# Kernel tuning notes

Hardware: AMD Instinct MI355X
Metric: run time of the kernel (lower is better)

Reference implementation:

```python
import jax, jax.numpy as jnp
import numpy as np

M, K, N = 4096, 4096, 11008  # tokens, in_features, out_features
PACK = 8  # int4 nibbles per int32


def setup_inputs() -> dict:
    key = jax.random.key(0)
    k1, k2, k3, k4, k5 = jax.random.split(key, 5)
    x = jax.random.normal(k1, (M, K), dtype=jnp.float32)
    weights = jax.random.randint(k2, (N, K // PACK), 0, 2147483647, dtype=jnp.int32)
    # positive per-channel scales, small float zero offsets (GPTQ-style affine)
    scales = jax.random.uniform(k3, (N,), dtype=jnp.float32, minval=0.005, maxval=0.02)
    zeros = jax.random.normal(k4, (N,), dtype=jnp.float32) * 0.05
    bias = jax.random.normal(k5, (N,), dtype=jnp.float32) * 0.02
    return {"x": x, "weights": weights, "scales": scales, "zeros": zeros, "bias": bias}


def _unpack_int4(weights):
    # weights: [N, K//8] int32 -> nibbles [N, K] in [0, 15]
    shifts = jnp.arange(PACK, dtype=jnp.int32) * 4  # [8]
    nib = (weights[:, :, None] >> shifts[None, None, :]) & 0xF  # [N, K//8, 8]
    return nib.reshape(weights.shape[0], -1)  # [N, K]


def reference(x, weights, scales, zeros, bias):
    x_dtype = x.dtype
    xb = x.astype(jnp.bfloat16)
    q = _unpack_int4(weights).astype(jnp.bfloat16)  # [N, K]
    # dequant: w = q * scale + zero  (per output channel)
    w = q * scales.astype(jnp.bfloat16)[:, None] + zeros.astype(jnp.bfloat16)[:, None]
    out = jnp.einsum('mk,nk->mn', xb, w, preferred_element_type=jnp.float32)
    out = out + bias[None, :]
    return out.astype(x_dtype)
```

## Files before the change

kernel.cpp:

```cpp
#include <hip/hip_runtime.h>
#include <stdint.h>

#define MDIM 4096
#define KDIM 4096
#define NDIM 11008
#define KP   (KDIM/8)
#define NQB  (NDIM*KP/256)

typedef float  f32x4   __attribute__((ext_vector_type(4)));
typedef __bf16 bf16x8  __attribute__((ext_vector_type(8)));
typedef unsigned short u16x8 __attribute__((ext_vector_type(8)));
typedef int    i32x4   __attribute__((ext_vector_type(4)));
typedef int    i32x16  __attribute__((ext_vector_type(16)));
typedef char   c8x8    __attribute__((ext_vector_type(8)));
typedef char   c8x16   __attribute__((ext_vector_type(16)));

__device__ __forceinline__ unsigned short f2bf(float f) {
  uint32_t u = __builtin_bit_cast(uint32_t, f);
  u += 0x7FFFu + ((u >> 16) & 1u);
  return (unsigned short)(u >> 16);
}
__device__ __forceinline__ float bf2f(unsigned short h) {
  return __builtin_bit_cast(float, (uint32_t)h << 16);
}
__device__ __forceinline__ float bf16r(float f) { return bf2f(f2bf(f)); }

__device__ __forceinline__ void lds16(const void* g, void* l) {
  __builtin_amdgcn_global_load_lds(
      (const __attribute__((address_space(1))) unsigned int*)g,
      (__attribute__((address_space(3))) unsigned int*)l, 16, 0, 0);
}

__global__ __launch_bounds__(256) void prepass_kernel(
    const uint32_t* __restrict__ wq, c8x8* __restrict__ Q8,
    const float* __restrict__ x, c8x16* __restrict__ X8,
    float* __restrict__ delta, float* __restrict__ xsum) {
  __shared__ float red[256];
  const int blk = blockIdx.x, t = threadIdx.x;
  if (blk < NQB) {
    int idx = blk * 256 + t;
    uint32_t w = wq[idx];
    c8x8 v;
#pragma unroll
    for (int j = 0; j < 8; ++j) v[j] = (char)((w >> (4 * j)) & 0xF);
    Q8[idx] = v;
    return;
  }
  const int row = blk - NQB;
  const float4* xr = (const float4*)(x + (size_t)row * KDIM);
  float xb[16];
#pragma unroll
  for (int i = 0; i < 4; ++i) {
    float4 f = xr[t * 4 + i];
    xb[i * 4 + 0] = bf16r(f.x); xb[i * 4 + 1] = bf16r(f.y);
    xb[i * 4 + 2] = bf16r(f.z); xb[i * 4 + 3] = bf16r(f.w);
  }
  float mx = 0.f, sm = 0.f;
#pragma unroll
  for (int j = 0; j < 16; ++j) { mx = fmaxf(mx, fabsf(xb[j])); sm += xb[j]; }
  red[t] = mx; __syncthreads();
  for (int o = 128; o > 0; o >>= 1) {
    if (t < o) red[t] = fmaxf(red[t], red[t + o]);
    __syncthreads();
  }
  const float rmx = red[0];
  __syncthreads();
  red[t] = sm; __syncthreads();
  for (int o = 128; o > 0; o >>= 1) {
    if (t < o) red[t] += red[t + o];
    __syncthreads();
  }
  const float rsm = red[0];
  const float inv = (rmx > 0.f) ? 127.0f / rmx : 0.f;
  if (t == 0) {
    delta[row] = (rmx > 0.f) ? rmx / 127.0f : 0.f;
    xsum[row]  = rsm;
  }
  c8x16 q;
#pragma unroll
  for (int j = 0; j < 16; ++j) q[j] = (char)__float2int_rn(xb[j] * inv);
  X8[(size_t)row * 256 + t] = q;
}

__global__ __launch_bounds__(512, 2) void gemm256_i8_kernel(
    const char* __restrict__ A8, const char* __restrict__ Q8,
    const float* __restrict__ delta, const float* __restrict__ xsum,
    const float* __restrict__ scales, const float* __restrict__ zeros,
    const float* __restrict__ bias, float* __restrict__ out) {
  __shared__ __align__(16) char smem[131072];

  const int tid  = threadIdx.x;
  const int lane = tid & 63;
  const int wave = tid >> 6;
  const int wm   = wave >> 2;
  const int wn   = wave & 3;

  const int b   = blockIdx.x;
  const int swz = (b & 7) * 86 + (b >> 3);
  const int mt  = swz / 43;
  const int nt  = swz - mt * 43;
  const int bm0 = mt * 256, bn0 = nt * 256;

  const int srow   = lane >> 2;
  const int schunk = lane & 3;
  const int perm0  = schunk ^ (((srow >> 3) & 1) << 1);
  const int perm1  = perm0 ^ 1;
  const char* aR  = A8 + (size_t)(bm0 + wave * 32 + srow) * KDIM + perm0 * 16;
  const char* aR2 = A8 + (size_t)(bm0 + wave * 32 + 16 + srow) * KDIM + perm1 * 16;
  const char* bR  = Q8 + (size_t)(bn0 + wave * 32 + srow) * KDIM + perm0 * 16;
  const char* bR2 = Q8 + (size_t)(bn0 + wave * 32 + 16 + srow) * KDIM + perm1 * 16;

  const int r31 = lane & 31;
  const int sub = r31 >> 4;
  const int r15 = r31 & 15;
  const int hk  = lane >> 5;
  const int rd0 = sub * 1024 + r15 * 64 + ((hk ^ sub) << 4) + ((r15 & 8) << 2);
  const int rd1 = rd0 ^ 32;

  const int aoffc = wm * 8192;
  const int boffc = 65536 + wn * 4096;

  i32x16 acc[4][2];
#pragma unroll
  for (int i = 0; i < 4; ++i)
#pragma unroll
    for (int j = 0; j < 2; ++j)
#pragma unroll
      for (int r = 0; r < 16; ++r) acc[i][j][r] = 0;

  i32x4 Af[4], Bf[2];

#define STAGE_A(tile, h, slot)                                              \
  do {                                                                      \
    const size_t ko_ = (size_t)((tile) * 128 + (h) * 64);                   \
    char* d_ = smem + ((slot) << 14) + wave * 2048;                         \
    lds16(aR + ko_, d_);                                                    \
    lds16(aR2 + ko_, d_ + 1024);                                            \
  } while (0)

#define STAGE_B(tile, h, slot)                                              \
  do {                                                                      \
    const size_t ko_ = (size_t)((tile) * 128 + (h) * 64);                   \
    char* d_ = smem + 65536 + ((slot) << 14) + wave * 2048;                 \
    lds16(bR + ko_, d_);                                                    \
    lds16(bR2 + ko_, d_ + 1024);                                            \
  } while (0)

#define READ6(slotbase, S)                                                  \
  do {                                                                      \
    const int ro_ = (S) ? rd1 : rd0;                                        \
    _Pragma("unroll") for (int mf = 0; mf < 4; ++mf)                        \
        Af[mf] = *(const i32x4*)(smem + aoffc + (slotbase) +                \
                                 mf * 2048 + ro_);                          \
    _Pragma("unroll") for (int nf = 0; nf < 2; ++nf)                        \
        Bf[nf] = *(const i32x4*)(smem + boffc + (slotbase) +                \
                                 nf * 2048 + ro_);                          \
  } while (0)

#define MFMA8()                                                             \
  __builtin_amdgcn_s_setprio(1);                                            \
  _Pragma("unroll") for (int mf = 0; mf < 4; ++mf)                          \
      _Pragma("unroll") for (int nf = 0; nf < 2; ++nf)                      \
          acc[mf][nf] = __builtin_amdgcn_mfma_i32_32x32x32_i8(              \
              Af[mf], Bf[nf], acc[mf][nf], 0, 0, 0);                        \
  __builtin_amdgcn_s_setprio(0);

#define BAR                                                                 \
  __builtin_amdgcn_s_barrier();                                             \
  __builtin_amdgcn_sched_barrier(0);

#define VMWAIT(N) asm volatile("s_waitcnt vmcnt(" #N ")" ::: "memory")

#define TILE(T, S0s, S1s, SN1s, NSTG, VM1STMT, VM3STMT)                     \
  do {                                                                      \
    READ6((S0s) << 14, 0);                                                  \
    if ((NSTG) >= 1) STAGE_A((T) + 1, 1, SN1s);                             \
    BAR; MFMA8(); BAR;                                                      \
    READ6((S0s) << 14, 1);                                                  \
    if ((NSTG) >= 2) STAGE_B((T) + 1, 1, SN1s);                             \
    VM1STMT;                                                                \
    BAR; MFMA8(); BAR;                                                      \
    READ6((S1s) << 14, 0);                                                  \
    if ((NSTG) >= 3) STAGE_A((T) + 2, 0, S0s);                              \
    BAR; MFMA8(); BAR;                                                      \
    READ6((S1s) << 14, 1);                                                  \
    if ((NSTG) >= 4) STAGE_B((T) + 2, 0, S0s);                              \
    VM3STMT;                                                                \
    BAR; MFMA8(); BAR;                                                      \
  } while (0)

  STAGE_A(0, 0, 0);
  STAGE_B(0, 0, 0);
  STAGE_A(0, 1, 1);
  STAGE_B(0, 1, 1);
  STAGE_A(1, 0, 2);
  STAGE_B(1, 0, 2);
  VMWAIT(8);
  BAR;

  for (int tt = 0; tt < 30; tt += 2) {
    TILE(tt,     0, 1, 3, 4, VMWAIT(8), VMWAIT(8));
    TILE(tt + 1, 2, 3, 1, 4, VMWAIT(8), VMWAIT(8));
  }
  TILE(30, 0, 1, 3, 2, VMWAIT(8), VMWAIT(4));
  TILE(31, 2, 3, 1, 0, VMWAIT(0), (void)0);

#undef TILE
#undef VMWAIT
#undef BAR
#undef MFMA8
#undef READ6
#undef STAGE_B
#undef STAGE_A

  const int colv = bn0 + wn * 64 + (lane & 31);
  const int rowb = bm0 + wm * 128 + ((lane >> 5) << 2);
  float sb[2], zb[2], bv[2];
#pragma unroll
  for (int nf = 0; nf < 2; ++nf) {
    sb[nf] = bf16r(scales[colv + nf * 32]);
    zb[nf] = bf16r(zeros[colv + nf * 32]);
    bv[nf] = bias[colv + nf * 32];
  }
#pragma unroll
  for (int mf = 0; mf < 4; ++mf)
#pragma unroll
    for (int reg = 0; reg < 16; ++reg) {
      const int row = rowb + mf * 32 + (reg & 3) + ((reg >> 2) << 3);
      const float dm = delta[row];
      const float xm = xsum[row];
#pragma unroll
      for (int nf = 0; nf < 2; ++nf)
        out[(size_t)row * NDIM + colv + nf * 32] =
            (float)acc[mf][nf][reg] * (dm * sb[nf]) + (zb[nf] * xm + bv[nf]);
    }
}

__global__ __launch_bounds__(256, 3) void gemm_fused_kernel(
    const float* __restrict__ x, const uint32_t* __restrict__ wq,
    const float* __restrict__ scales, const float* __restrict__ zeros,
    const float* __restrict__ bias, float* __restrict__ out) {
  __shared__ __align__(16) char smem[2 * 128 * 64 * 2];
  char* As = smem;
  char* Bs = smem + 16384;

  const int tid  = threadIdx.x;
  const int lane = tid & 63;
  const int wave = tid >> 6;
  const int wm = wave >> 1, wn = wave & 1;

  const int b   = blockIdx.x;
  const int swz = (b & 7) * 344 + (b >> 3);
  const int mt  = swz / 86;
  const int nt  = swz - mt * 86;
  const int bm0 = mt * 128, bn0 = nt * 128;

  f32x4 acc[4][4];
#pragma unroll
  for (int i = 0; i < 4; ++i)
#pragma unroll
    for (int j = 0; j < 4; ++j) acc[i][j] = (f32x4){0.f, 0.f, 0.f, 0.f};

  const int base_a = ((wm * 64 + (lane & 15)) << 7) + ((lane >> 4) << 4);
  const int base_b = ((wn * 64 + (lane & 15)) << 7) + ((lane >> 4) << 4);

  float sv[4], zv[4];
#pragma unroll
  for (int it = 0; it < 4; ++it) {
    int r = bn0 + it * 32 + (tid >> 3);
    sv[it] = bf16r(scales[r]);
    zv[it] = bf16r(zeros[r]);
  }

  for (int kt = 0; kt < KDIM / 64; ++kt) {
    const int k0 = kt * 64;
    __syncthreads();
#pragma unroll
    for (int it = 0; it < 4; ++it) {
      int ch = it * 256 + tid;
      int row = ch >> 3, c8 = ch & 7;
      const float* src = x + (size_t)(bm0 + row) * KDIM + k0 + c8 * 8;
      float4 f0 = *(const float4*)src;
      float4 f1 = *(const float4*)(src + 4);
      u16x8 v;
      v[0] = f2bf(f0.x); v[1] = f2bf(f0.y); v[2] = f2bf(f0.z); v[3] = f2bf(f0.w);
      v[4] = f2bf(f1.x); v[5] = f2bf(f1.y); v[6] = f2bf(f1.z); v[7] = f2bf(f1.w);
      *(u16x8*)(As + row * 128 + c8 * 16) = v;
    }
#pragma unroll
    for (int it = 0; it < 4; ++it) {
      int ch = it * 256 + tid;
      int row = ch >> 3, kp = ch & 7;
      uint32_t w = wq[(size_t)(bn0 + row) * KP + kt * 8 + kp];
      float s = sv[it], z = zv[it];
      u16x8 v;
#pragma unroll
      for (int j = 0; j < 8; ++j) {
        float qf = (float)((w >> (4 * j)) & 0xF);
        float t  = bf16r(qf * s);
        v[j] = f2bf(t + z);
      }
      *(u16x8*)(Bs + row * 128 + kp * 16) = v;
    }
    __syncthreads();
#pragma unroll
    for (int ks = 0; ks < 2; ++ks) {
      bf16x8 af[4], bf[4];
#pragma unroll
      for (int i = 0; i < 4; ++i)
        af[i] = *(const bf16x8*)(As + base_a + i * 2048 + ks * 64);
#pragma unroll
      for (int j = 0; j < 4; ++j)
        bf[j] = *(const bf16x8*)(Bs + base_b + j * 2048 + ks * 64);
#pragma unroll
      for (int i = 0; i < 4; ++i)
#pragma unroll
        for (int j = 0; j < 4; ++j)
          acc[i][j] = __builtin_amdgcn_mfma_f32_16x16x32_bf16(af[i], bf[j],
                                                              acc[i][j], 0, 0, 0);
    }
  }

  const int colbase = bn0 + wn * 64 + (lane & 15);
  const int rowbase = bm0 + wm * 64 + ((lane >> 4) << 2);
  float bv[4];
#pragma unroll
  for (int j = 0; j < 4; ++j) bv[j] = bias[colbase + j * 16];
#pragma unroll
  for (int i = 0; i < 4; ++i) {
#pragma unroll
    for (int j = 0; j < 4; ++j) {
      size_t base = (size_t)(rowbase + i * 16) * NDIM + colbase + j * 16;
#pragma unroll
      for (int r = 0; r < 4; ++r)
        out[base + (size_t)r * NDIM] = acc[i][j][r] + bv[j];
    }
  }
}

extern "C" void kernel_launch(void* const* d_in, const int* in_sizes, int n_in,
                              void* d_out, int out_size, void* d_ws, size_t ws_size,
                              hipStream_t stream) {
  const float*    x      = (const float*)d_in[0];
  const uint32_t* wq     = (const uint32_t*)d_in[1];
  const float*    scales = (const float*)d_in[2];
  const float*    zeros  = (const float*)d_in[3];
  const float*    bias   = (const float*)d_in[4];
  float*          out    = (float*)d_out;

  const size_t offQ = 0;
  const size_t szQ  = (size_t)NDIM * KDIM;
  const size_t offX = szQ;
  const size_t szX  = (size_t)MDIM * KDIM;
  const size_t offD = offX + szX;
  const size_t offS = offD + MDIM * sizeof(float);
  const size_t need = offS + MDIM * sizeof(float);

  if (ws_size >= need) {
    char*  Q8    = (char*)d_ws + offQ;
    char*  X8    = (char*)d_ws + offX;
    float* dlt   = (float*)((char*)d_ws + offD);
    float* xsm   = (float*)((char*)d_ws + offS);
    prepass_kernel<<<NQB + MDIM, 256, 0, stream>>>(wq, (c8x8*)Q8, x,
                                                   (c8x16*)X8, dlt, xsm);
    gemm256_i8_kernel<<<688, 512, 0, stream>>>(X8, Q8, dlt, xsm, scales, zeros,
                                               bias, out);
  } else {
    gemm_fused_kernel<<<2752, 256, 0, stream>>>(x, wq, scales, zeros, bias, out);
  }
}
```

Baseline: 229.3 us.

## Pre-swizzle int8 operands into MFMA fragment layout and load directly to registers

The prepass now writes both the quantized activations and the unpacked weights in a fragment-major layout, where each 1 KB block holds one 32x32 int8 MFMA operand fragment indexed by lane. The GEMM kernel drops the LDS staging, the swizzled LDS reads and the block-wide barriers. Each wave instead issues 16-byte global loads straight into registers, double-buffered, with vmcnt waits. This removes LDS traffic and barrier stalls, but waves in a block no longer share staged tiles, so L2/global read traffic per block rises several-fold and latency hiding depends only on the two-deep register prefetch.

```diff
diff --git a/kernel.cpp b/kernel.cpp
--- a/kernel.cpp
+++ b/kernel.cpp
@@ -5,7 +5,8 @@
 #define KDIM 4096
 #define NDIM 11008
 #define KP   (KDIM/8)
-#define NQB  (NDIM*KP/256)
+#define NQB  (NDIM/32*32)
+#define QBLK ((NDIM/32)*32)
 
 typedef float  f32x4   __attribute__((ext_vector_type(4)));
 typedef __bf16 bf16x8  __attribute__((ext_vector_type(8)));
@@ -25,28 +26,28 @@
 }
 __device__ __forceinline__ float bf16r(float f) { return bf2f(f2bf(f)); }
 
-__device__ __forceinline__ void lds16(const void* g, void* l) {
-  __builtin_amdgcn_global_load_lds(
-      (const __attribute__((address_space(1))) unsigned int*)g,
-      (__attribute__((address_space(3))) unsigned int*)l, 16, 0, 0);
-}
-
 __global__ __launch_bounds__(256) void prepass_kernel(
-    const uint32_t* __restrict__ wq, c8x8* __restrict__ Q8,
-    const float* __restrict__ x, c8x16* __restrict__ X8,
+    const uint32_t* __restrict__ wq, char* __restrict__ Q8f,
+    const float* __restrict__ x, char* __restrict__ X8f,
     float* __restrict__ delta, float* __restrict__ xsum) {
   __shared__ float red[256];
   const int blk = blockIdx.x, t = threadIdx.x;
-  if (blk < NQB) {
-    int idx = blk * 256 + t;
-    uint32_t w = wq[idx];
-    c8x8 v;
-#pragma unroll
-    for (int j = 0; j < 8; ++j) v[j] = (char)((w >> (4 * j)) & 0xF);
-    Q8[idx] = v;
+  if (blk < QBLK) {
+    const int n32 = blk >> 5, kg = blk & 31;
+    const int r = t & 31, half = (t >> 5) & 1, j = t >> 6;
+    const int k32 = kg * 4 + j;
+    const uint32_t* src = wq + (size_t)(n32 * 32 + r) * KP + k32 * 4 + half * 2;
+    const uint32_t w0 = src[0], w1 = src[1];
+    c8x16 v;
+#pragma unroll
+    for (int i = 0; i < 8; ++i) {
+      v[i]     = (char)((w0 >> (4 * i)) & 0xF);
+      v[8 + i] = (char)((w1 >> (4 * i)) & 0xF);
+    }
+    *(c8x16*)(Q8f + ((size_t)n32 * 128 + k32) * 1024 + (r + 32 * half) * 16) = v;
     return;
   }
-  const int row = blk - NQB;
+  const int row = blk - QBLK;
   const float4* xr = (const float4*)(x + (size_t)row * KDIM);
   float xb[16];
 #pragma unroll
@@ -79,16 +80,15 @@
   c8x16 q;
 #pragma unroll
   for (int j = 0; j < 16; ++j) q[j] = (char)__float2int_rn(xb[j] * inv);
-  X8[(size_t)row * 256 + t] = q;
-}
-
-__global__ __launch_bounds__(512, 2) void gemm256_i8_kernel(
-    const char* __restrict__ A8, const char* __restrict__ Q8,
+  const int lane16 = (row & 31) + 32 * (t & 1);
+  *(c8x16*)(X8f + ((size_t)(row >> 5) * 128 + (t >> 1)) * 1024 + lane16 * 16) = q;
+}
+
+__global__ __launch_bounds__(512, 2) void gemm_i8f_kernel(
+    const char* __restrict__ X8f, const char* __restrict__ Q8f,
     const float* __restrict__ delta, const float* __restrict__ xsum,
     const float* __restrict__ scales, const float* __restrict__ zeros,
     const float* __restrict__ bias, float* __restrict__ out) {
-  __shared__ __align__(16) char smem[131072];
-
   const int tid  = threadIdx.x;
   const int lane = tid & 63;
   const int wave = tid >> 6;
@@ -101,24 +101,10 @@
   const int nt  = swz - mt * 43;
   const int bm0 = mt * 256, bn0 = nt * 256;
 
-  const int srow   = lane >> 2;
-  const int schunk = lane & 3;
-  const int perm0  = schunk ^ (((srow >> 3) & 1) << 1);
-  const int perm1  = perm0 ^ 1;
-  const char* aR  = A8 + (size_t)(bm0 + wave * 32 + srow) * KDIM + perm0 * 16;
-  const char* aR2 = A8 + (size_t)(bm0 + wave * 32 + 16 + srow) * KDIM + perm1 * 16;
-  const char* bR  = Q8 + (size_t)(bn0 + wave * 32 + srow) * KDIM + perm0 * 16;
-  const char* bR2 = Q8 + (size_t)(bn0 + wave * 32 + 16 + srow) * KDIM + perm1 * 16;
-
-  const int r31 = lane & 31;
-  const int sub = r31 >> 4;
-  const int r15 = r31 & 15;
-  const int hk  = lane >> 5;
-  const int rd0 = sub * 1024 + r15 * 64 + ((hk ^ sub) << 4) + ((r15 & 8) << 2);
-  const int rd1 = rd0 ^ 32;
-
-  const int aoffc = wm * 8192;
-  const int boffc = 65536 + wn * 4096;
+  const char* aB = X8f + ((size_t)((bm0 >> 5) + wm * 4) * 128) * 1024
+                       + (size_t)lane * 16;
+  const char* bB = Q8f + ((size_t)((bn0 >> 5) + wn * 2) * 128) * 1024
+                       + (size_t)lane * 16;
 
   i32x16 acc[4][2];
 #pragma unroll
@@ -128,90 +114,45 @@
 #pragma unroll
       for (int r = 0; r < 16; ++r) acc[i][j][r] = 0;
 
-  i32x4 Af[4], Bf[2];
-
-#define STAGE_A(tile, h, slot)                                              \
+  i32x4 A0[4], B0[2], A1[4], B1[2];
+
+#define LOADSET(AS, BS, K)                                                  \
   do {                                                                      \
-    const size_t ko_ = (size_t)((tile) * 128 + (h) * 64);                   \
-    char* d_ = smem + ((slot) << 14) + wave * 2048;                         \
-    lds16(aR + ko_, d_);                                                    \
-    lds16(aR2 + ko_, d_ + 1024);                                            \
+    const size_t ko_ = (size_t)(K) * 1024;                                  \
+    _Pragma("unroll") for (int mf = 0; mf < 4; ++mf)                        \
+        AS[mf] = *(const i32x4*)(aB + (size_t)mf * 131072 + ko_);           \
+    _Pragma("unroll") for (int nf = 0; nf < 2; ++nf)                        \
+        BS[nf] = *(const i32x4*)(bB + (size_t)nf * 131072 + ko_);           \
   } while (0)
 
-#define STAGE_B(tile, h, slot)                                              \
-  do {                                                                      \
-    const size_t ko_ = (size_t)((tile) * 128 + (h) * 64);                   \
-    char* d_ = smem + 65536 + ((slot) << 14) + wave * 2048;                 \
-    lds16(bR + ko_, d_);                                                    \
-    lds16(bR2 + ko_, d_ + 1024);                                            \
-  } while (0)
-
-#define READ6(slotbase, S)                                                  \
-  do {                                                                      \
-    const int ro_ = (S) ? rd1 : rd0;                                        \
-    _Pragma("unroll") for (int mf = 0; mf < 4; ++mf)                        \
-        Af[mf] = *(const i32x4*)(smem + aoffc + (slotbase) +                \
-                                 mf * 2048 + ro_);                          \
-    _Pragma("unroll") for (int nf = 0; nf < 2; ++nf)                        \
-        Bf[nf] = *(const i32x4*)(smem + boffc + (slotbase) +                \
-                                 nf * 2048 + ro_);                          \
-  } while (0)
-
-#define MFMA8()                                                             \
+#define MFMA8(AS, BS)                                                       \
   __builtin_amdgcn_s_setprio(1);                                            \
   _Pragma("unroll") for (int mf = 0; mf < 4; ++mf)                          \
       _Pragma("unroll") for (int nf = 0; nf < 2; ++nf)                      \
           acc[mf][nf] = __builtin_amdgcn_mfma_i32_32x32x32_i8(              \
-              Af[mf], Bf[nf], acc[mf][nf], 0, 0, 0);                        \
+              AS[mf], BS[nf], acc[mf][nf], 0, 0, 0);                        \
   __builtin_amdgcn_s_setprio(0);
 
-#define BAR                                                                 \
-  __builtin_amdgcn_s_barrier();                                             \
-  __builtin_amdgcn_sched_barrier(0);
-
 #define VMWAIT(N) asm volatile("s_waitcnt vmcnt(" #N ")" ::: "memory")
 
-#define TILE(T, S0s, S1s, SN1s, NSTG, VM1STMT, VM3STMT)                     \
-  do {                                                                      \
-    READ6((S0s) << 14, 0);                                                  \
-    if ((NSTG) >= 1) STAGE_A((T) + 1, 1, SN1s);                             \
-    BAR; MFMA8(); BAR;                                                      \
-    READ6((S0s) << 14, 1);                                                  \
-    if ((NSTG) >= 2) STAGE_B((T) + 1, 1, SN1s);                             \
-    VM1STMT;                                                                \
-    BAR; MFMA8(); BAR;                                                      \
-    READ6((S1s) << 14, 0);                                                  \
-    if ((NSTG) >= 3) STAGE_A((T) + 2, 0, S0s);                              \
-    BAR; MFMA8(); BAR;                                                      \
-    READ6((S1s) << 14, 1);                                                  \
-    if ((NSTG) >= 4) STAGE_B((T) + 2, 0, S0s);                              \
-    VM3STMT;                                                                \
-    BAR; MFMA8(); BAR;                                                      \
-  } while (0)
-
-  STAGE_A(0, 0, 0);
-  STAGE_B(0, 0, 0);
-  STAGE_A(0, 1, 1);
-  STAGE_B(0, 1, 1);
-  STAGE_A(1, 0, 2);
-  STAGE_B(1, 0, 2);
-  VMWAIT(8);
-  BAR;
-
-  for (int tt = 0; tt < 30; tt += 2) {
-    TILE(tt,     0, 1, 3, 4, VMWAIT(8), VMWAIT(8));
-    TILE(tt + 1, 2, 3, 1, 4, VMWAIT(8), VMWAIT(8));
-  }
-  TILE(30, 0, 1, 3, 2, VMWAIT(8), VMWAIT(4));
-  TILE(31, 2, 3, 1, 0, VMWAIT(0), (void)0);
-
-#undef TILE
+  LOADSET(A0, B0, 0);
+  LOADSET(A1, B1, 1);
+  for (int k = 0; k < 126; k += 2) {
+    VMWAIT(6);
+    MFMA8(A0, B0);
+    LOADSET(A0, B0, k + 2);
+    VMWAIT(6);
+    MFMA8(A1, B1);
+    LOADSET(A1, B1, k + 3);
+  }
+  VMWAIT(6);
+  MFMA8(A0, B0);
+  VMWAIT(0);
+  MFMA8(A1, B1);
+
 #undef VMWAIT
-#undef BAR
 #undef MFMA8
-#undef READ6
-#undef STAGE_B
-#undef STAGE_A
+#undef LOADSET
 
   const int colv = bn0 + wn * 64 + (lane & 31);
   const int rowb = bm0 + wm * 128 + ((lane >> 5) << 2);
@@ -357,14 +298,13 @@
   const size_t need = offS + MDIM * sizeof(float);
 
   if (ws_size >= need) {
-    char*  Q8    = (char*)d_ws + offQ;
-    char*  X8    = (char*)d_ws + offX;
+    char*  Q8f   = (char*)d_ws + offQ;
+    char*  X8f   = (char*)d_ws + offX;
     float* dlt   = (float*)((char*)d_ws + offD);
     float* xsm   = (float*)((char*)d_ws + offS);
-    prepass_kernel<<<NQB + MDIM, 256, 0, stream>>>(wq, (c8x8*)Q8, x,
-                                                   (c8x16*)X8, dlt, xsm);
-    gemm256_i8_kernel<<<688, 512, 0, stream>>>(X8, Q8, dlt, xsm, scales, zeros,
-                                               bias, out);
+    prepass_kernel<<<QBLK + MDIM, 256, 0, stream>>>(wq, Q8f, x, X8f, dlt, xsm);
+    gemm_i8f_kernel<<<688, 512, 0, stream>>>(X8f, Q8f, dlt, xsm, scales, zeros,
+                                             bias, out);
   } else {
     gemm_fused_kernel<<<2752, 256, 0, stream>>>(x, wq, scales, zeros, bias, out);
   }
```

Measured after the change: 273.9 us. +19.4%, slower.
